# Performance work log

Hardware: AMD Instinct MI355X
Metric: run time of the kernel (lower is better)

Reference implementation:

```python
import jax, jax.numpy as jnp
import numpy as np

WS = 7  # window size
NH = 4  # num heads


def _relative_position_index(ws: int) -> np.ndarray:
    coords = np.stack(np.meshgrid(np.arange(ws), np.arange(ws), indexing='ij'))  # [2,ws,ws]
    coords = coords.reshape(2, -1)
    rel = coords[:, :, None] - coords[:, None, :]  # [2,N,N]
    rel = rel.transpose(1, 2, 0) + (ws - 1)
    rel[:, :, 0] *= 2 * ws - 1
    return rel.sum(-1)  # [N,N] in [0,(2ws-1)^2)


REL_IDX = _relative_position_index(WS)


def setup_inputs() -> dict:
    key = jax.random.key(0)
    k1, k2, k3, k4 = jax.random.split(key, 4)
    dim = 128
    x = jax.random.normal(k1, (64, 56, 56, dim), dtype=jnp.float32)
    qkv_w = jax.random.normal(k2, (dim, 3 * dim), dtype=jnp.float32) * (dim ** -0.5)
    qkv_b = jnp.zeros((3 * dim,), dtype=jnp.float32)
    proj_w = jax.random.normal(k3, (dim, dim), dtype=jnp.float32) * (dim ** -0.5)
    proj_b = jnp.zeros((dim,), dtype=jnp.float32)
    bias_table = jax.random.truncated_normal(k4, -2.0, 2.0, ((2 * WS - 1) ** 2, NH), dtype=jnp.float32) * 0.02
    return {"x": x, "qkv_w": qkv_w, "qkv_b": qkv_b, "proj_w": proj_w, "proj_b": proj_b, "bias_table": bias_table}


def reference(x, qkv_w, qkv_b, proj_w, proj_b, bias_table):
    B, H, W, C = x.shape
    ws, nh = WS, NH
    hd = C // nh
    N = ws * ws
    # window partition: [B*nWh*nWw, N, C]  (H,W divisible by ws -> no padding branch)
    xw = x.reshape(B, H // ws, ws, W // ws, ws, C).transpose(0, 1, 3, 2, 4, 5).reshape(-1, N, C)
    qkv = xw @ qkv_w + qkv_b  # [nW, N, 3C]
    qkv = qkv.reshape(-1, N, 3, nh, hd).transpose(2, 0, 3, 1, 4)  # [3, nW, nh, N, hd]
    q, k, v = qkv[0], qkv[1], qkv[2]
    attn = jnp.einsum('whqd,whkd->whqk', q, k) * (hd ** -0.5)  # [nW, nh, N, N]
    rel_bias = bias_table[REL_IDX.reshape(-1)].reshape(N, N, nh).transpose(2, 0, 1)  # [nh,N,N]
    attn = jax.nn.softmax(attn + rel_bias[None], axis=-1)
    out = jnp.einsum('whqk,whkd->whqd', attn, v)  # [nW, nh, N, hd]
    out = out.transpose(0, 2, 1, 3).reshape(-1, N, C)
    out = out @ proj_w + proj_b
    # window reverse
    out = out.reshape(B, H // ws, W // ws, ws, ws, C).transpose(0, 1, 3, 2, 4, 5).reshape(B, H, W, C)
    return out
```

## Files before the change

### kernel.cpp

```cpp
#include <hip/hip_runtime.h>
#include <hip/hip_bf16.h>

#define NTOK 49
#define NPAD 64
#define CDIM 128
#define C3   384
#define NHEAD 4
#define HDIM 32
#define SCALE 0.17677669529663687f

#define QS 136
#define VS 72
#define PS 72

typedef __attribute__((ext_vector_type(8))) __bf16 bf16x8;
typedef __attribute__((ext_vector_type(4))) __bf16 bf16x4;
typedef __attribute__((ext_vector_type(4))) float f32x4;

#define PIN(v) asm volatile("" : "+v"(v))


__global__ __launch_bounds__(256) void prep_kernel(
    const float* __restrict__ qkv_w, const float* __restrict__ proj_w,
    const float* __restrict__ bias_table,
    __bf16* __restrict__ qkvT, __bf16* __restrict__ projT, float* __restrict__ blut)
{
  int o = blockIdx.x * 256 + threadIdx.x;
  if (o < CDIM * C3) {
    int n = o >> 7, k = o & 127;
    float v = qkv_w[k * C3 + n];
    if (n < CDIM) v *= SCALE;
    qkvT[o] = (__bf16)v;
  } else if (o < CDIM * C3 + CDIM * CDIM) {
    int o2 = o - CDIM * C3;
    int n = o2 >> 7, k = o2 & 127;
    projT[o2] = (__bf16)proj_w[k * CDIM + n];
  } else if (o < CDIM * C3 + CDIM * CDIM + NHEAD * NPAD * NPAD) {
    int t3 = o - (CDIM * C3 + CDIM * CDIM);
    int h = t3 >> 12, r = (t3 >> 6) & 63, c = t3 & 63;
    float v;
    if (c >= NTOK) v = -1e30f;
    else if (r >= NTOK) v = 0.0f;
    else {
      int idx = (r / 7 - c / 7 + 6) * 13 + (r % 7 - c % 7 + 6);
      v = bias_table[idx * NHEAD + h];
    }
    blut[t3] = v;
  }
}

__global__ __launch_bounds__(512, 4) void attn_kernel(
    const float* __restrict__ x, const float* __restrict__ qkv_b,
    const float* __restrict__ proj_b,
    const __bf16* __restrict__ qkvT, const __bf16* __restrict__ projT,
    const float* __restrict__ blut, float* __restrict__ out)
{
  __shared__ __align__(16) char smem[71680];
  __bf16* qs_ = (__bf16*)smem;
  __bf16* ks_ = qs_ + NPAD * QS;
  __bf16* vT_ = ks_ + NPAD * QS;
  char*   un_ = (char*)(vT_ + CDIM * VS);
  __bf16* xa_ = (__bf16*)un_;
  __bf16* Pm_ = (__bf16*)un_;

  const int tid  = threadIdx.x;
  const int wave = tid >> 6;
  const int lane = tid & 63;
  const int l15  = lane & 15;
  const int lg   = lane >> 4;

  const int win = blockIdx.x;
  const int b  = win >> 6;
  const int wh = (win >> 3) & 7;
  const int ww = win & 7;
  const float* xbase = x + (((b * 56) + wh * 7) * 56 + ww * 7) * CDIM;

  #pragma unroll
  for (int p = 0; p < 2; ++p) {
    int L = p * 512 + tid;
    int r = L >> 4, c = L & 15;
    bf16x8 v8;
    if (r < NTOK) {
      const float* g = xbase + ((r / 7) * 56 + (r % 7)) * CDIM + c * 8;
      f32x4 x0 = *(const f32x4*)g;
      f32x4 x1 = *(const f32x4*)(g + 4);
      v8[0] = (__bf16)x0[0]; v8[1] = (__bf16)x0[1]; v8[2] = (__bf16)x0[2]; v8[3] = (__bf16)x0[3];
      v8[4] = (__bf16)x1[0]; v8[5] = (__bf16)x1[1]; v8[6] = (__bf16)x1[2]; v8[7] = (__bf16)x1[3];
    } else {
      #pragma unroll
      for (int q2 = 0; q2 < 8; ++q2) v8[q2] = (__bf16)0.0f;
    }
    *(bf16x8*)(xa_ + r * QS + c * 8) = v8;
  }

  const int nb = wave * 48;
  bf16x8 bq[3][4];
  #pragma unroll
  for (int nt = 0; nt < 3; ++nt)
    #pragma unroll
    for (int kt = 0; kt < 4; ++kt) {
      bq[nt][kt] = *(const bf16x8*)(qkvT + (nb + nt * 16 + l15) * CDIM + kt * 32 + lg * 8);
      PIN(bq[nt][kt]);
    }
  float qb[3];
  #pragma unroll
  for (int nt = 0; nt < 3; ++nt) {
    qb[nt] = qkv_b[nb + nt * 16 + l15];
    if (nb + nt * 16 < CDIM) qb[nt] *= SCALE;
  }

  __syncthreads();

  #pragma unroll 2
  for (int mt = 0; mt < 4; ++mt) {
    bf16x8 a[4];
    #pragma unroll
    for (int kt = 0; kt < 4; ++kt)
      a[kt] = *(const bf16x8*)(xa_ + (mt * 16 + l15) * QS + kt * 32 + lg * 8);

    f32x4 acc[3];
    #pragma unroll
    for (int nt = 0; nt < 3; ++nt) { acc[nt][0]=0.f; acc[nt][1]=0.f; acc[nt][2]=0.f; acc[nt][3]=0.f; }
    #pragma unroll
    for (int nt = 0; nt < 3; ++nt)
      #pragma unroll
      for (int kt = 0; kt < 4; ++kt)
        acc[nt] = __builtin_amdgcn_mfma_f32_16x16x32_bf16(a[kt], bq[nt][kt], acc[nt], 0, 0, 0);

    const int r0 = mt * 16 + lg * 4;
    #pragma unroll
    for (int nt = 0; nt < 3; ++nt) {
      const int n = nb + nt * 16 + l15;
      if (n < CDIM) {
        #pragma unroll
        for (int i = 0; i < 4; ++i)
          qs_[(r0 + i) * QS + n] = (__bf16)(acc[nt][i] + qb[nt]);
      } else if (n < 2 * CDIM) {
        #pragma unroll
        for (int i = 0; i < 4; ++i)
          ks_[(r0 + i) * QS + (n - CDIM)] = (__bf16)(acc[nt][i] + qb[nt]);
      } else {
        bf16x4 vv;
        #pragma unroll
        for (int i = 0; i < 4; ++i) vv[i] = (__bf16)(acc[nt][i] + qb[nt]);
        *(bf16x4*)(vT_ + (n - 2 * CDIM) * VS + r0) = vv;
      }
    }
  }
  __syncthreads();

  const int nb2 = wave * 16;
  bf16x8 bp[4];
  #pragma unroll
  for (int kt = 0; kt < 4; ++kt) {
    bp[kt] = *(const bf16x8*)(projT + (nb2 + l15) * CDIM + kt * 32 + lg * 8);
    PIN(bp[kt]);
  }
  const float pb = proj_b[nb2 + l15];

  __bf16* O_ = qs_;

  {
    const int h  = wave & 3;
    const int hc = h * HDIM;
    const float* blh = blut + h * 4096;
    __bf16* Pw = Pm_ + wave * 16 * PS;

    bf16x8 bk[4];
    #pragma unroll
    for (int nt = 0; nt < 4; ++nt)
      bk[nt] = *(const bf16x8*)(ks_ + (nt * 16 + l15) * QS + hc + lg * 8);
    bf16x8 bv[2][2];
    #pragma unroll
    for (int n16 = 0; n16 < 2; ++n16)
      #pragma unroll
      for (int kt = 0; kt < 2; ++kt)
        bv[n16][kt] = *(const bf16x8*)(vT_ + (hc + n16 * 16 + l15) * VS + kt * 32 + lg * 8);

    #pragma unroll
    for (int mi = 0; mi < 2; ++mi) {
      const int mt = (wave >> 2) * 2 + mi;
      const int m0 = mt * 16;

      float bias[4][4];
      #pragma unroll
      for (int i = 0; i < 4; ++i) {
        const int r = m0 + lg * 4 + i;
        #pragma unroll
        for (int c = 0; c < 4; ++c) bias[i][c] = blh[r * 64 + c * 16 + l15];
      }

      bf16x8 aqf = *(const bf16x8*)(qs_ + (m0 + l15) * QS + hc + lg * 8);
      f32x4 s[4];
      #pragma unroll
      for (int nt = 0; nt < 4; ++nt) {
        f32x4 z; z[0]=0.f; z[1]=0.f; z[2]=0.f; z[3]=0.f;
        s[nt] = __builtin_amdgcn_mfma_f32_16x16x32_bf16(aqf, bk[nt], z, 0, 0, 0);
      }
      float inv[4];
      #pragma unroll
      for (int i = 0; i < 4; ++i) {
        const int lr = lg * 4 + i;
        float e0 = __expf(s[0][i] + bias[i][0]);
        float e1 = __expf(s[1][i] + bias[i][1]);
        float e2 = __expf(s[2][i] + bias[i][2]);
        float e3 = __expf(s[3][i] + bias[i][3]);
        Pw[lr * PS +      l15] = (__bf16)e0;
        Pw[lr * PS + 16 + l15] = (__bf16)e1;
        Pw[lr * PS + 32 + l15] = (__bf16)e2;
        Pw[lr * PS + 48 + l15] = (__bf16)e3;
        float sum = (e0 + e1) + (e2 + e3);
        #pragma unroll
        for (int off = 1; off < 16; off <<= 1) sum += __shfl_xor(sum, off);
        inv[i] = __builtin_amdgcn_rcpf(sum);
      }
      f32x4 o0, o1;
      o0[0]=0.f;o0[1]=0.f;o0[2]=0.f;o0[3]=0.f; o1[0]=0.f;o1[1]=0.f;o1[2]=0.f;o1[3]=0.f;
      #pragma unroll
      for (int kt = 0; kt < 2; ++kt) {
        bf16x8 ap = *(const bf16x8*)(Pw + l15 * PS + kt * 32 + lg * 8);
        o0 = __builtin_amdgcn_mfma_f32_16x16x32_bf16(ap, bv[0][kt], o0, 0, 0, 0);
        o1 = __builtin_amdgcn_mfma_f32_16x16x32_bf16(ap, bv[1][kt], o1, 0, 0, 0);
      }
      const int r0 = m0 + lg * 4;
      #pragma unroll
      for (int i = 0; i < 4; ++i) {
        O_[(r0 + i) * QS + hc +      l15] = (__bf16)(o0[i] * inv[i]);
        O_[(r0 + i) * QS + hc + 16 + l15] = (__bf16)(o1[i] * inv[i]);
      }
    }
  }
  __syncthreads();

  float* outw = out + (((b * 56) + wh * 7) * 56 + ww * 7) * CDIM;
  #pragma unroll
  for (int mt = 0; mt < 4; ++mt) {
    bf16x8 ao[4];
    #pragma unroll
    for (int kt = 0; kt < 4; ++kt)
      ao[kt] = *(const bf16x8*)(O_ + (mt * 16 + l15) * QS + kt * 32 + lg * 8);
    f32x4 c0;
    c0[0]=0.f;c0[1]=0.f;c0[2]=0.f;c0[3]=0.f;
    #pragma unroll
    for (int kt = 0; kt < 4; ++kt)
      c0 = __builtin_amdgcn_mfma_f32_16x16x32_bf16(ao[kt], bp[kt], c0, 0, 0, 0);
    #pragma unroll
    for (int i = 0; i < 4; ++i) {
      const int r = mt * 16 + lg * 4 + i;
      if (r < NTOK) {
        float* po = outw + ((r / 7) * 56 + (r % 7)) * CDIM + nb2;
        po[l15] = c0[i] + pb;
      }
    }
  }
}

extern "C" void kernel_launch(void* const* d_in, const int* in_sizes, int n_in,
                              void* d_out, int out_size, void* d_ws, size_t ws_size,
                              hipStream_t stream) {
  const float* x          = (const float*)d_in[0];
  const float* qkv_w      = (const float*)d_in[1];
  const float* qkv_b      = (const float*)d_in[2];
  const float* proj_w     = (const float*)d_in[3];
  const float* proj_b     = (const float*)d_in[4];
  const float* bias_table = (const float*)d_in[5];

  __bf16* qkvT  = (__bf16*)d_ws;
  __bf16* projT = qkvT + C3 * CDIM;
  float*  blut  = (float*)((char*)d_ws + 131072);
  float*  out   = (float*)d_out;

  hipLaunchKernelGGL(prep_kernel, dim3(320), dim3(256), 0, stream,
                     qkv_w, proj_w, bias_table, qkvT, projT, blut);
  hipLaunchKernelGGL(attn_kernel, dim3(4096), dim3(512), 0, stream,
                     x, qkv_b, proj_b, qkvT, projT, blut, out);
}
```

Before: 267.3 us.

## Load x directly into MFMA fragments, reuse K buffer for P, compute S transposed

Drops the shared-memory staging of x by loading and converting the fp32 window rows straight into MFMA A fragments, with padded rows clamped. The probability tile is written into the K region after K and V fragments are pulled into registers, so the separate scratch buffer goes away and shared memory shrinks. The launch bound occupancy target rises from four to six blocks. Scores are computed transposed (K as A, Q as B) with a transposed bias LUT, so the row-sum reduction needs two cross-lane shuffles plus a broadcast instead of four shuffles per row. The cost is redundant global x loads per wave, an extra barrier, and added register pressure from the pinned K and V fragments.

```diff
diff --git a/kernel.cpp b/kernel.cpp
--- a/kernel.cpp
+++ b/kernel.cpp
@@ -11,7 +11,6 @@
 
 #define QS 136
 #define VS 72
-#define PS 72
 
 typedef __attribute__((ext_vector_type(8))) __bf16 bf16x8;
 typedef __attribute__((ext_vector_type(4))) __bf16 bf16x4;
@@ -23,7 +22,7 @@
 __global__ __launch_bounds__(256) void prep_kernel(
     const float* __restrict__ qkv_w, const float* __restrict__ proj_w,
     const float* __restrict__ bias_table,
-    __bf16* __restrict__ qkvT, __bf16* __restrict__ projT, float* __restrict__ blut)
+    __bf16* __restrict__ qkvT, __bf16* __restrict__ projT, float* __restrict__ blutT)
 {
   int o = blockIdx.x * 256 + threadIdx.x;
   if (o < CDIM * C3) {
@@ -37,31 +36,28 @@
     projT[o2] = (__bf16)proj_w[k * CDIM + n];
   } else if (o < CDIM * C3 + CDIM * CDIM + NHEAD * NPAD * NPAD) {
     int t3 = o - (CDIM * C3 + CDIM * CDIM);
-    int h = t3 >> 12, r = (t3 >> 6) & 63, c = t3 & 63;
+    int h = t3 >> 12, k = (t3 >> 6) & 63, q = t3 & 63;
     float v;
-    if (c >= NTOK) v = -1e30f;
-    else if (r >= NTOK) v = 0.0f;
+    if (k >= NTOK) v = -1e30f;
+    else if (q >= NTOK) v = 0.0f;
     else {
-      int idx = (r / 7 - c / 7 + 6) * 13 + (r % 7 - c % 7 + 6);
+      int idx = (q / 7 - k / 7 + 6) * 13 + (q % 7 - k % 7 + 6);
       v = bias_table[idx * NHEAD + h];
     }
-    blut[t3] = v;
+    blutT[t3] = v;
   }
 }
 
-__global__ __launch_bounds__(512, 4) void attn_kernel(
+__global__ __launch_bounds__(512, 6) void attn_kernel(
     const float* __restrict__ x, const float* __restrict__ qkv_b,
     const float* __restrict__ proj_b,
     const __bf16* __restrict__ qkvT, const __bf16* __restrict__ projT,
-    const float* __restrict__ blut, float* __restrict__ out)
+    const float* __restrict__ blutT, float* __restrict__ out)
 {
-  __shared__ __align__(16) char smem[71680];
+  __shared__ __align__(16) char smem[53248];
   __bf16* qs_ = (__bf16*)smem;
   __bf16* ks_ = qs_ + NPAD * QS;
   __bf16* vT_ = ks_ + NPAD * QS;
-  char*   un_ = (char*)(vT_ + CDIM * VS);
-  __bf16* xa_ = (__bf16*)un_;
-  __bf16* Pm_ = (__bf16*)un_;
 
   const int tid  = threadIdx.x;
   const int wave = tid >> 6;
@@ -75,24 +71,6 @@
   const int ww = win & 7;
   const float* xbase = x + (((b * 56) + wh * 7) * 56 + ww * 7) * CDIM;
 
-  #pragma unroll
-  for (int p = 0; p < 2; ++p) {
-    int L = p * 512 + tid;
-    int r = L >> 4, c = L & 15;
-    bf16x8 v8;
-    if (r < NTOK) {
-      const float* g = xbase + ((r / 7) * 56 + (r % 7)) * CDIM + c * 8;
-      f32x4 x0 = *(const f32x4*)g;
-      f32x4 x1 = *(const f32x4*)(g + 4);
-      v8[0] = (__bf16)x0[0]; v8[1] = (__bf16)x0[1]; v8[2] = (__bf16)x0[2]; v8[3] = (__bf16)x0[3];
-      v8[4] = (__bf16)x1[0]; v8[5] = (__bf16)x1[1]; v8[6] = (__bf16)x1[2]; v8[7] = (__bf16)x1[3];
-    } else {
-      #pragma unroll
-      for (int q2 = 0; q2 < 8; ++q2) v8[q2] = (__bf16)0.0f;
-    }
-    *(bf16x8*)(xa_ + r * QS + c * 8) = v8;
-  }
-
   const int nb = wave * 48;
   bf16x8 bq[3][4];
   #pragma unroll
@@ -109,15 +87,21 @@
     if (nb + nt * 16 < CDIM) qb[nt] *= SCALE;
   }
 
-  __syncthreads();
-
-  #pragma unroll 2
+  #pragma unroll 1
   for (int mt = 0; mt < 4; ++mt) {
+    const int t  = mt * 16 + l15;
+    const int tc = t < NTOK ? t : NTOK - 1;
+    const float* src = xbase + ((tc / 7) * 56 + (tc % 7)) * CDIM + lg * 8;
     bf16x8 a[4];
     #pragma unroll
-    for (int kt = 0; kt < 4; ++kt)
-      a[kt] = *(const bf16x8*)(xa_ + (mt * 16 + l15) * QS + kt * 32 + lg * 8);
-
+    for (int kt = 0; kt < 4; ++kt) {
+      f32x4 x0 = *(const f32x4*)(src + kt * 32);
+      f32x4 x1 = *(const f32x4*)(src + kt * 32 + 4);
+      bf16x8 av;
+      av[0] = (__bf16)x0[0]; av[1] = (__bf16)x0[1]; av[2] = (__bf16)x0[2]; av[3] = (__bf16)x0[3];
+      av[4] = (__bf16)x1[0]; av[5] = (__bf16)x1[1]; av[6] = (__bf16)x1[2]; av[7] = (__bf16)x1[3];
+      a[kt] = av;
+    }
     f32x4 acc[3];
     #pragma unroll
     for (int nt = 0; nt < 3; ++nt) { acc[nt][0]=0.f; acc[nt][1]=0.f; acc[nt][2]=0.f; acc[nt][3]=0.f; }
@@ -149,6 +133,90 @@
   }
   __syncthreads();
 
+  const int h  = wave & 3;
+  const int hc = h * HDIM;
+  const int mh = wave >> 2;
+  const float* bTh = blutT + h * 4096;
+
+  bf16x8 bk[4];
+  #pragma unroll
+  for (int nt = 0; nt < 4; ++nt) {
+    bk[nt] = *(const bf16x8*)(ks_ + (nt * 16 + l15) * QS + hc + lg * 8);
+    PIN(bk[nt]);
+  }
+  bf16x8 bv[2][2];
+  #pragma unroll
+  for (int n16 = 0; n16 < 2; ++n16)
+    #pragma unroll
+    for (int kt2 = 0; kt2 < 2; ++kt2) {
+      bv[n16][kt2] = *(const bf16x8*)(vT_ + (hc + n16 * 16 + l15) * VS + kt2 * 32 + lg * 8);
+      PIN(bv[n16][kt2]);
+    }
+  __syncthreads();
+
+  __bf16* O_ = qs_;
+  __bf16* Pw = ks_ + wave * 16 * QS;
+
+  #pragma unroll
+  for (int mi = 0; mi < 2; ++mi) {
+    const int m0 = (mh * 2 + mi) * 16;
+
+    float bias[4][4];
+    #pragma unroll
+    for (int nt = 0; nt < 4; ++nt)
+      #pragma unroll
+      for (int i = 0; i < 4; ++i)
+        bias[nt][i] = bTh[(nt * 16 + lg * 4 + i) * 64 + m0 + l15];
+
+    bf16x8 qB = *(const bf16x8*)(qs_ + (m0 + l15) * QS + hc + lg * 8);
+    f32x4 s[4];
+    #pragma unroll
+    for (int nt = 0; nt < 4; ++nt) {
+      f32x4 z; z[0]=0.f; z[1]=0.f; z[2]=0.f; z[3]=0.f;
+      s[nt] = __builtin_amdgcn_mfma_f32_16x16x32_bf16(bk[nt], qB, z, 0, 0, 0);
+    }
+    float e[4][4];
+    #pragma unroll
+    for (int nt = 0; nt < 4; ++nt)
+      #pragma unroll
+      for (int i = 0; i < 4; ++i)
+        e[nt][i] = __expf(s[nt][i] + bias[nt][i]);
+
+    #pragma unroll
+    for (int nt = 0; nt < 4; ++nt) {
+      bf16x4 p4;
+      p4[0] = (__bf16)e[nt][0]; p4[1] = (__bf16)e[nt][1];
+      p4[2] = (__bf16)e[nt][2]; p4[3] = (__bf16)e[nt][3];
+      *(bf16x4*)(Pw + l15 * QS + nt * 16 + lg * 4) = p4;
+    }
+
+    float sum = ((e[0][0]+e[0][1])+(e[0][2]+e[0][3])) + ((e[1][0]+e[1][1])+(e[1][2]+e[1][3]))
+              + ((e[2][0]+e[2][1])+(e[2][2]+e[2][3])) + ((e[3][0]+e[3][1])+(e[3][2]+e[3][3]));
+    sum += __shfl_xor(sum, 16);
+    sum += __shfl_xor(sum, 32);
+    const float inv = __builtin_amdgcn_rcpf(sum);
+
+    float invT[4];
+    #pragma unroll
+    for (int i = 0; i < 4; ++i) invT[i] = __shfl(inv, lg * 4 + i);
+
+    f32x4 o0, o1;
+    o0[0]=0.f;o0[1]=0.f;o0[2]=0.f;o0[3]=0.f; o1[0]=0.f;o1[1]=0.f;o1[2]=0.f;o1[3]=0.f;
+    #pragma unroll
+    for (int kt2 = 0; kt2 < 2; ++kt2) {
+      bf16x8 ap = *(const bf16x8*)(Pw + l15 * QS + kt2 * 32 + lg * 8);
+      o0 = __builtin_amdgcn_mfma_f32_16x16x32_bf16(ap, bv[0][kt2], o0, 0, 0, 0);
+      o1 = __builtin_amdgcn_mfma_f32_16x16x32_bf16(ap, bv[1][kt2], o1, 0, 0, 0);
+    }
+    const int r0 = m0 + lg * 4;
+    #pragma unroll
+    for (int i = 0; i < 4; ++i) {
+      O_[(r0 + i) * QS + hc +      l15] = (__bf16)(o0[i] * invT[i]);
+      O_[(r0 + i) * QS + hc + 16 + l15] = (__bf16)(o1[i] * invT[i]);
+    }
+  }
+  __syncthreads();
+
   const int nb2 = wave * 16;
   bf16x8 bp[4];
   #pragma unroll
@@ -157,82 +225,8 @@
     PIN(bp[kt]);
   }
   const float pb = proj_b[nb2 + l15];
-
-  __bf16* O_ = qs_;
-
-  {
-    const int h  = wave & 3;
-    const int hc = h * HDIM;
-    const float* blh = blut + h * 4096;
-    __bf16* Pw = Pm_ + wave * 16 * PS;
-
-    bf16x8 bk[4];
-    #pragma unroll
-    for (int nt = 0; nt < 4; ++nt)
-      bk[nt] = *(const bf16x8*)(ks_ + (nt * 16 + l15) * QS + hc + lg * 8);
-    bf16x8 bv[2][2];
-    #pragma unroll
-    for (int n16 = 0; n16 < 2; ++n16)
-      #pragma unroll
-      for (int kt = 0; kt < 2; ++kt)
-        bv[n16][kt] = *(const bf16x8*)(vT_ + (hc + n16 * 16 + l15) * VS + kt * 32 + lg * 8);
-
-    #pragma unroll
-    for (int mi = 0; mi < 2; ++mi) {
-      const int mt = (wave >> 2) * 2 + mi;
-      const int m0 = mt * 16;
-
-      float bias[4][4];
-      #pragma unroll
-      for (int i = 0; i < 4; ++i) {
-        const int r = m0 + lg * 4 + i;
-        #pragma unroll
-        for (int c = 0; c < 4; ++c) bias[i][c] = blh[r * 64 + c * 16 + l15];
-      }
-
-      bf16x8 aqf = *(const bf16x8*)(qs_ + (m0 + l15) * QS + hc + lg * 8);
-      f32x4 s[4];
-      #pragma unroll
-      for (int nt = 0; nt < 4; ++nt) {
-        f32x4 z; z[0]=0.f; z[1]=0.f; z[2]=0.f; z[3]=0.f;
-        s[nt] = __builtin_amdgcn_mfma_f32_16x16x32_bf16(aqf, bk[nt], z, 0, 0, 0);
-      }
-      float inv[4];
-      #pragma unroll
-      for (int i = 0; i < 4; ++i) {
-        const int lr = lg * 4 + i;
-        float e0 = __expf(s[0][i] + bias[i][0]);
-        float e1 = __expf(s[1][i] + bias[i][1]);
-        float e2 = __expf(s[2][i] + bias[i][2]);
-        float e3 = __expf(s[3][i] + bias[i][3]);
-        Pw[lr * PS +      l15] = (__bf16)e0;
-        Pw[lr * PS + 16 + l15] = (__bf16)e1;
-        Pw[lr * PS + 32 + l15] = (__bf16)e2;
-        Pw[lr * PS + 48 + l15] = (__bf16)e3;
-        float sum = (e0 + e1) + (e2 + e3);
-        #pragma unroll
-        for (int off = 1; off < 16; off <<= 1) sum += __shfl_xor(sum, off);
-        inv[i] = __builtin_amdgcn_rcpf(sum);
-      }
-      f32x4 o0, o1;
-      o0[0]=0.f;o0[1]=0.f;o0[2]=0.f;o0[3]=0.f; o1[0]=0.f;o1[1]=0.f;o1[2]=0.f;o1[3]=0.f;
-      #pragma unroll
-      for (int kt = 0; kt < 2; ++kt) {
-        bf16x8 ap = *(const bf16x8*)(Pw + l15 * PS + kt * 32 + lg * 8);
-        o0 = __builtin_amdgcn_mfma_f32_16x16x32_bf16(ap, bv[0][kt], o0, 0, 0, 0);
-        o1 = __builtin_amdgcn_mfma_f32_16x16x32_bf16(ap, bv[1][kt], o1, 0, 0, 0);
-      }
-      const int r0 = m0 + lg * 4;
-      #pragma unroll
-      for (int i = 0; i < 4; ++i) {
-        O_[(r0 + i) * QS + hc +      l15] = (__bf16)(o0[i] * inv[i]);
-        O_[(r0 + i) * QS + hc + 16 + l15] = (__bf16)(o1[i] * inv[i]);
-      }
-    }
-  }
-  __syncthreads();
-
   float* outw = out + (((b * 56) + wh * 7) * 56 + ww * 7) * CDIM;
+
   #pragma unroll
   for (int mt = 0; mt < 4; ++mt) {
     bf16x8 ao[4];
@@ -267,11 +261,11 @@
 
   __bf16* qkvT  = (__bf16*)d_ws;
   __bf16* projT = qkvT + C3 * CDIM;
-  float*  blut  = (float*)((char*)d_ws + 131072);
+  float*  blutT = (float*)((char*)d_ws + 131072);
   float*  out   = (float*)d_out;
 
   hipLaunchKernelGGL(prep_kernel, dim3(320), dim3(256), 0, stream,
-                     qkv_w, proj_w, bias_table, qkvT, projT, blut);
+                     qkv_w, proj_w, bias_table, qkvT, projT, blutT);
   hipLaunchKernelGGL(attn_kernel, dim3(4096), dim3(512), 0, stream,
-                     x, qkv_b, proj_b, qkvT, projT, blut, out);
+                     x, qkv_b, proj_b, qkvT, projT, blutT, out);
 }
```

New measurement: 456.6 us. 1.71x slower.
